# Optimization experiments

Hardware: AMD Instinct MI355X
Metric: run time of the kernel (lower is better)

The kernel has to match this reference:

```python
import jax, jax.numpy as jnp
import numpy as np

B, TA, TV, D, H = 4, 1024, 1024, 512, 8
HD = D // H
SCALE = HD ** -0.5
LN_EPS = 1e-5


def setup_inputs() -> dict:
    key = jax.random.key(0)
    ks = jax.random.split(key, 16)
    init = lambda k, shape, s: (jax.random.normal(k, shape, jnp.float32) * s)
    inp = {
        'q': jax.random.normal(ks[0], (B, TA, D), jnp.float32),
        'k': jax.random.normal(ks[1], (B, TV, D), jnp.float32),
        'v': jax.random.normal(ks[2], (B, TV, D), jnp.float32),
        'guide_map': jax.random.uniform(ks[3], (B, TA, TV), jnp.float32),
        'Wq': init(ks[4], (D, D), D ** -0.5), 'bq': jnp.zeros((D,), jnp.float32),
        'Wk': init(ks[5], (D, D), D ** -0.5), 'bk': jnp.zeros((D,), jnp.float32),
        'Wv': init(ks[6], (D, D), D ** -0.5), 'bv': jnp.zeros((D,), jnp.float32),
        'Wo': init(ks[7], (D, D), D ** -0.5), 'bo': jnp.zeros((D,), jnp.float32),
        'ln_gamma': jnp.ones((D,), jnp.float32),
        'ln_beta': jnp.zeros((D,), jnp.float32),
        'gate': jnp.zeros((1,), jnp.float32),
        'bias_scale': jnp.array(10.0, jnp.float32),
    }
    return inp


def layer_norm(x, gamma, beta):
    mu = jnp.mean(x, axis=-1, keepdims=True)
    var = jnp.mean(jnp.square(x - mu), axis=-1, keepdims=True)
    return (x - mu) * jax.lax.rsqrt(var + LN_EPS) * gamma + beta


def reference(q, k, v, guide_map, Wq, bq, Wk, bk, Wv, bv, Wo, bo, ln_gamma, ln_beta, gate, bias_scale):
    # project and split heads: [B, H, T, hd]
    Q = (q @ Wq.T + bq).reshape(B, TA, H, HD).transpose(0, 2, 1, 3)
    K = (k @ Wk.T + bk).reshape(B, TV, H, HD).transpose(0, 2, 1, 3)
    V = (v @ Wv.T + bv).reshape(B, TV, H, HD).transpose(0, 2, 1, 3)
    scores = jnp.einsum('bhqd,bhkd->bhqk', Q, K) * SCALE
    # transport bias, broadcast over heads (guide_map is [B,Ta,Tv])
    transport_bias = jnp.log(guide_map + 1e-8) * jax.nn.softplus(bias_scale)
    scores = scores + transport_bias[:, None, :, :]
    attn = jax.nn.softmax(scores, axis=-1)  # dropout is identity in eval
    context = jnp.einsum('bhqk,bhkd->bhqd', attn, V)
    context = context.transpose(0, 2, 1, 3).reshape(B, TA, D)
    out = context @ Wo.T + bo
    return layer_norm(q + jax.nn.sigmoid(gate) * out, ln_gamma, ln_beta)
```

## Files before the change

kernel.cpp:

```cpp
#include <hip/hip_runtime.h>
#include <hip/hip_bf16.h>
#include <math.h>

typedef __bf16 bf16_t;
typedef _Float16 hf16_t;
typedef bf16_t bf16x8 __attribute__((ext_vector_type(8)));
typedef hf16_t hf16x8 __attribute__((ext_vector_type(8)));
typedef float f32x4 __attribute__((ext_vector_type(4)));

#define B_  4
#define TA_ 1024
#define TV_ 1024
#define D_  512
#define H_  8
#define HD_ 64
#define SCALE_ 0.125f

__device__ inline void g2l16(const void* g, void* l) {
    __builtin_amdgcn_global_load_lds(
        (const __attribute__((address_space(1))) void*)g,
        (__attribute__((address_space(3))) void*)l, 16, 0, 0);
}

template <int CTRL>
__device__ inline float dppmov(float x) {
    int xi = __float_as_int(x);
    return __int_as_float(__builtin_amdgcn_update_dpp(xi, xi, CTRL, 0xF, 0xF, false));
}
__device__ inline float row16_max(float x) {
    x = fmaxf(x, dppmov<0xB1>(x));
    x = fmaxf(x, dppmov<0x4E>(x));
    x = fmaxf(x, dppmov<0x141>(x));
    x = fmaxf(x, dppmov<0x140>(x));
    return x;
}
__device__ inline float row16_sum(float x) {
    x += dppmov<0xB1>(x);
    x += dppmov<0x4E>(x);
    x += dppmov<0x141>(x);
    x += dppmov<0x140>(x);
    return x;
}

__global__ __launch_bounds__(256) void prep_all(
    const float* __restrict__ G, hf16_t* __restrict__ bias_t,
    const float* __restrict__ q, const float* __restrict__ k, const float* __restrict__ v,
    const float* __restrict__ Wq, const float* __restrict__ Wk,
    const float* __restrict__ Wv, const float* __restrict__ Wo,
    bf16_t* __restrict__ qb, bf16_t* __restrict__ kb, bf16_t* __restrict__ vb,
    bf16_t* __restrict__ Wb)
{
    const int tid = threadIdx.x;
    if (blockIdx.x < 1024) {
        __shared__ float Gt[64][68];
        const int kt = blockIdx.x & 15, q64 = (blockIdx.x >> 4) & 15, b = blockIdx.x >> 8;
        const int row = tid >> 4, col4 = (tid & 15) * 4;
        #pragma unroll
        for (int it = 0; it < 4; ++it) {
            int r = it * 16 + row;
            f32x4 g = *(const f32x4*)(G + ((size_t)(b * TA_ + q64 * 64 + r)) * TV_ + kt * 64 + col4);
            *(f32x4*)&Gt[r][col4] = g;
        }
        __syncthreads();
        const int lane = tid & 63, wave = tid >> 6, quad = lane >> 4, l16 = lane & 15;
        hf16x8 lo, hi;
        #pragma unroll
        for (int ct = 0; ct < 4; ++ct) {
            #pragma unroll
            for (int r = 0; r < 4; ++r) {
                float gv = Gt[wave * 16 + quad * 4 + r][ct * 16 + l16];
                float lb = __logf(gv + 1e-8f);
                int idx = ct * 4 + r;
                if (idx < 8) lo[idx] = (hf16_t)lb; else hi[idx - 8] = (hf16_t)lb;
            }
        }
        size_t doff = ((((size_t)b * 16 + kt) * 16 + q64) * 256 + tid) * 16;
        *(hf16x8*)(bias_t + doff) = lo;
        *(hf16x8*)(bias_t + doff + 8) = hi;
    } else {
        const size_t i = ((size_t)(blockIdx.x - 1024) * 256 + tid) * 8;
        const float* src; bf16_t* dst; size_t off;
        const size_t M2 = (size_t)1 << 21;
        if (i < M2)          { src = q; dst = qb; off = i; }
        else if (i < 2 * M2) { src = k; dst = kb; off = i - M2; }
        else if (i < 3 * M2) { src = v; dst = vb; off = i - 2 * M2; }
        else {
            size_t j = i - 3 * M2;
            int wsel = (int)(j >> 18); off = j & 262143;
            src = (wsel == 0) ? Wq : (wsel == 1) ? Wk : (wsel == 2) ? Wv : Wo;
            dst = Wb + ((size_t)wsel << 18);
        }
        f32x4 a = *(const f32x4*)(src + off), c = *(const f32x4*)(src + off + 4);
        bf16x8 r;
        #pragma unroll
        for (int t = 0; t < 4; ++t) { r[t] = (bf16_t)a[t]; r[t + 4] = (bf16_t)c[t]; }
        *(bf16x8*)(dst + off) = r;
    }
}

__device__ inline void gemm128_core(
    const bf16_t* __restrict__ X, const bf16_t* __restrict__ W,
    int mbase, int nbase, bf16_t (*__restrict__ Asm)[128 * 32],
    bf16_t (*__restrict__ Bsm)[128 * 32], f32x4 acc[4][4])
{
    const int tid  = threadIdx.x;
    const int wave = tid >> 6, lane = tid & 63;
    const int quad = lane >> 4, l16 = lane & 15;
    const int wm = wave & 1, wn = wave >> 1;
    const int srow = lane >> 2;
    const int scol = (lane & 3) * 8;

    auto stage = [&](int kt, int buf) {
        const int k0 = kt * 32;
        #pragma unroll
        for (int i = 0; i < 2; ++i) {
            const int row = wave * 32 + i * 16;
            g2l16(X + (size_t)(mbase + row + srow) * D_ + k0 + scol,
                  &Asm[buf][row * 32] + (size_t)lane * 8);
            g2l16(W + (size_t)(nbase + row + srow) * D_ + k0 + scol,
                  &Bsm[buf][row * 32] + (size_t)lane * 8);
        }
    };

    stage(0, 0);
    __syncthreads();
    for (int kt = 0; kt < 16; ++kt) {
        const int buf = kt & 1;
        if (kt < 15) stage(kt + 1, buf ^ 1);
        bf16x8 af[4], bf_[4];
        #pragma unroll
        for (int t = 0; t < 4; ++t) {
            af[t]  = *(const bf16x8*)&Asm[buf][(wm * 64 + t * 16 + l16) * 32 + quad * 8];
            bf_[t] = *(const bf16x8*)&Bsm[buf][(wn * 64 + t * 16 + l16) * 32 + quad * 8];
        }
        #pragma unroll
        for (int mt = 0; mt < 4; ++mt) {
            #pragma unroll
            for (int nt = 0; nt < 4; ++nt)
                acc[mt][nt] = __builtin_amdgcn_mfma_f32_16x16x32_bf16(af[mt], bf_[nt], acc[mt][nt], 0, 0, 0);
        }
        __syncthreads();
    }
}

__global__ __launch_bounds__(256) void gemm_qkv(
    const bf16_t* __restrict__ qb, const bf16_t* __restrict__ kb, const bf16_t* __restrict__ vb,
    const bf16_t* __restrict__ Wb,
    const float* __restrict__ bq, const float* __restrict__ bk, const float* __restrict__ bv,
    bf16_t* __restrict__ Qp, bf16_t* __restrict__ Kp, bf16_t* __restrict__ Vt)
{
    __shared__ bf16_t Asm[2][128 * 32];
    __shared__ bf16_t Bsm[2][128 * 32];

    const int tid  = threadIdx.x;
    const int wave = tid >> 6, lane = tid & 63;
    const int quad = lane >> 4, l16 = lane & 15;
    const int wm = wave & 1, wn = wave >> 1;
    const int mbase = blockIdx.x * 128, nbase = blockIdx.y * 128;
    const int z = blockIdx.z;

    const bf16_t* X   = (z == 0) ? qb : (z == 1) ? kb : vb;
    const float* bias = (z == 0) ? bq : (z == 1) ? bk : bv;
    const bf16_t* W   = Wb + ((size_t)z << 18);

    f32x4 acc[4][4] = {};
    gemm128_core(X, W, mbase, nbase, Asm, Bsm, acc);

    bf16_t* out = (z == 0) ? Qp : (z == 1) ? Kp : Vt;
    #pragma unroll
    for (int mt = 0; mt < 4; ++mt) {
        #pragma unroll
        for (int nt = 0; nt < 4; ++nt) {
            #pragma unroll
            for (int r = 0; r < 4; ++r) {
                int m = mbase + wm * 64 + mt * 16 + quad * 4 + r;
                int n = nbase + wn * 64 + nt * 16 + l16;
                float val = acc[mt][nt][r] + bias[n];
                int b = m >> 10, t = m & 1023, h = n >> 6, hd = n & 63;
                if (z != 2)
                    out[(((size_t)(b * H_ + h) * TA_) + t) * HD_ + hd] = (bf16_t)val;
                else
                    out[((size_t)(b * H_ + h) * HD_ + hd) * TV_ + t] = (bf16_t)val;
            }
        }
    }
}

__global__ __launch_bounds__(256) void gemm_out(
    const bf16_t* __restrict__ ctx, const bf16_t* __restrict__ Wob,
    const float* __restrict__ bo, bf16_t* __restrict__ op)
{
    __shared__ bf16_t Asm[2][128 * 32];
    __shared__ bf16_t Bsm[2][128 * 32];

    const int tid  = threadIdx.x;
    const int wave = tid >> 6, lane = tid & 63;
    const int quad = lane >> 4, l16 = lane & 15;
    const int wm = wave & 1, wn = wave >> 1;
    const int mbase = blockIdx.x * 128, nbase = blockIdx.y * 128;

    f32x4 acc[4][4] = {};
    gemm128_core(ctx, Wob, mbase, nbase, Asm, Bsm, acc);

    #pragma unroll
    for (int mt = 0; mt < 4; ++mt) {
        #pragma unroll
        for (int nt = 0; nt < 4; ++nt) {
            #pragma unroll
            for (int r = 0; r < 4; ++r) {
                int m = mbase + wm * 64 + mt * 16 + quad * 4 + r;
                int n = nbase + wn * 64 + nt * 16 + l16;
                op[(size_t)m * D_ + n] = (bf16_t)(acc[mt][nt][r] + bo[n]);
            }
        }
    }
}

__global__ __launch_bounds__(256) void attn_kernel(
    const bf16_t* __restrict__ Qp, const bf16_t* __restrict__ Kp,
    const bf16_t* __restrict__ Vt, const hf16_t* __restrict__ bias_t,
    const float* __restrict__ bias_scale,
    bf16_t* __restrict__ Opart, float* __restrict__ mpart, float* __restrict__ lpart)
{
    __shared__ bf16_t Ksm[2][64][72];
    __shared__ bf16_t Vsm[2][64][72];
    __shared__ bf16_t Plds[4][16][72];

    const int tid  = threadIdx.x;
    const int wave = tid >> 6, lane = tid & 63;
    const int quad = lane >> 4, l16 = lane & 15;
    const int bh = blockIdx.x, b = bh >> 3;
    const int q64 = blockIdx.y;
    const int z = blockIdx.z;
    const int t0 = z * 8;
    const int qbase = q64 * 64 + wave * 16;
    const int rsub = lane >> 3, csub = lane & 7;

    const float sp = log1pf(__expf(bias_scale[0]));

    bf16x8 aq[2];
    #pragma unroll
    for (int s = 0; s < 2; ++s)
        aq[s] = *(const bf16x8*)(Qp + ((size_t)bh * TA_ + qbase + l16) * HD_ + s * 32 + quad * 8);

    f32x4 o[4] = {};
    float m_[4], l_[4];
    #pragma unroll
    for (int i = 0; i < 4; ++i) { m_[i] = -1e30f; l_[i] = 0.f; }

    auto issue_kv = [&](int kt, bf16x8 kr[2], bf16x8 vr[2]) {
        const int kbase = kt * 64;
        #pragma unroll
        for (int i = 0; i < 2; ++i) {
            int row = wave * 16 + i * 8 + rsub;
            kr[i] = *(const bf16x8*)(Kp + ((size_t)bh * TV_ + kbase + row) * HD_ + csub * 8);
            vr[i] = *(const bf16x8*)(Vt + ((size_t)bh * HD_ + row) * TV_ + kbase + csub * 8);
        }
    };
    auto write_kv = [&](int buf, bf16x8 kr[2], bf16x8 vr[2]) {
        #pragma unroll
        for (int i = 0; i < 2; ++i) {
            int row = wave * 16 + i * 8 + rsub;
            *(bf16x8*)&Ksm[buf][row][csub * 8] = kr[i];
            *(bf16x8*)&Vsm[buf][row][csub * 8] = vr[i];
        }
    };

    const hf16_t* bias_base = bias_t + (((size_t)b * 16 * 16 + q64) * 256 + tid) * 16;
    auto bias_ld = [&](int kt, hf16x8& lo, hf16x8& hi) {
        const hf16_t* bp = bias_base + (size_t)kt * 65536;
        lo = *(const hf16x8*)bp;
        hi = *(const hf16x8*)(bp + 8);
    };
    hf16x8 b0lo, b0hi, b1lo, b1hi;
    bias_ld(t0, b0lo, b0hi);
    bias_ld(t0 + 1, b1lo, b1hi);

    {
        bf16x8 kr[2], vr[2];
        issue_kv(t0, kr, vr);
        write_kv(0, kr, vr);
    }
    __syncthreads();

    auto tile_body = [&](int lk, int buf, hf16x8& slo, hf16x8& shi) {
        const int kt = t0 + lk;
        bf16x8 krn[2], vrn[2];
        if (lk < 7) issue_kv(kt + 1, krn, vrn);
        hf16x8 clo = slo, chi = shi;
        if (lk < 6) bias_ld(kt + 2, slo, shi);

        f32x4 st[4];
        #pragma unroll
        for (int ct = 0; ct < 4; ++ct) {
            f32x4 acc = {};
            #pragma unroll
            for (int s = 0; s < 2; ++s) {
                bf16x8 bk = *(const bf16x8*)&Ksm[buf][ct * 16 + l16][s * 32 + quad * 8];
                acc = __builtin_amdgcn_mfma_f32_16x16x32_bf16(aq[s], bk, acc, 0, 0, 0);
            }
            st[ct] = acc;
        }
        float sv[4][4], mx[4];
        #pragma unroll
        for (int r = 0; r < 4; ++r) mx[r] = -1e30f;
        #pragma unroll
        for (int ct = 0; ct < 4; ++ct) {
            #pragma unroll
            for (int r = 0; r < 4; ++r) {
                int idx = ct * 4 + r;
                float lb = (idx < 8) ? (float)clo[idx] : (float)chi[idx - 8];
                float val = fmaf(lb, sp, st[ct][r] * SCALE_);
                sv[ct][r] = val;
                mx[r] = fmaxf(mx[r], val);
            }
        }
        float alpha[4];
        #pragma unroll
        for (int r = 0; r < 4; ++r) {
            mx[r] = row16_max(mx[r]);
            float mn = fmaxf(m_[r], mx[r]);
            alpha[r] = __expf(m_[r] - mn);
            m_[r] = mn;
        }
        #pragma unroll
        for (int ct = 0; ct < 4; ++ct) {
            #pragma unroll
            for (int r = 0; r < 4; ++r)
                sv[ct][r] = __expf(sv[ct][r] - m_[r]);
        }
        #pragma unroll
        for (int r = 0; r < 4; ++r) {
            float lsum = row16_sum(sv[0][r] + sv[1][r] + sv[2][r] + sv[3][r]);
            l_[r] = l_[r] * alpha[r] + lsum;
        }
        #pragma unroll
        for (int ct = 0; ct < 4; ++ct) {
            #pragma unroll
            for (int r = 0; r < 4; ++r)
                Plds[wave][quad * 4 + r][ct * 16 + l16] = (bf16_t)sv[ct][r];
        }
        #pragma unroll
        for (int dt = 0; dt < 4; ++dt) {
            #pragma unroll
            for (int r = 0; r < 4; ++r) o[dt][r] *= alpha[r];
        }
        #pragma unroll
        for (int s = 0; s < 2; ++s) {
            bf16x8 ap = *(const bf16x8*)&Plds[wave][l16][s * 32 + quad * 8];
            #pragma unroll
            for (int dt = 0; dt < 4; ++dt) {
                bf16x8 bv = *(const bf16x8*)&Vsm[buf][dt * 16 + l16][s * 32 + quad * 8];
                o[dt] = __builtin_amdgcn_mfma_f32_16x16x32_bf16(ap, bv, o[dt], 0, 0, 0);
            }
        }
        if (lk < 7) write_kv(buf ^ 1, krn, vrn);
        __syncthreads();
    };

    #pragma unroll 1
    for (int kk = 0; kk < 8; kk += 2) {
        tile_body(kk,     0, b0lo, b0hi);
        tile_body(kk + 1, 1, b1lo, b1hi);
    }

    const size_t blk = (size_t)bh * 16 + q64;
    bf16x8 plo, phi;
    #pragma unroll
    for (int dt = 0; dt < 4; ++dt) {
        #pragma unroll
        for (int r = 0; r < 4; ++r) {
            int idx = dt * 4 + r;
            if (idx < 8) plo[idx] = (bf16_t)o[dt][r]; else phi[idx - 8] = (bf16_t)o[dt][r];
        }
    }
    size_t poff = (((size_t)z * 512 + blk) * 256 + tid) * 16;
    *(bf16x8*)(Opart + poff) = plo;
    *(bf16x8*)(Opart + poff + 8) = phi;
    if (l16 == 0) {
        #pragma unroll
        for (int r = 0; r < 4; ++r) {
            int row = wave * 16 + quad * 4 + r;
            mpart[((size_t)z * 512 + blk) * 64 + row] = m_[r];
            lpart[((size_t)z * 512 + blk) * 64 + row] = l_[r];
        }
    }
}

__global__ __launch_bounds__(256) void attn_combine(
    const bf16_t* __restrict__ Opart, const float* __restrict__ mpart,
    const float* __restrict__ lpart, bf16_t* __restrict__ ctx)
{
    const int tid  = threadIdx.x;
    const int wave = tid >> 6, lane = tid & 63;
    const int quad = lane >> 4, l16 = lane & 15;
    const int bh = blockIdx.x, b = bh >> 3, h = bh & 7;
    const int q64 = blockIdx.y;
    const size_t blk = (size_t)bh * 16 + q64;

    size_t p0 = (blk * 256 + tid) * 16;
    size_t p1 = (((size_t)512 + blk) * 256 + tid) * 16;
    bf16x8 a0 = *(const bf16x8*)(Opart + p0), a1 = *(const bf16x8*)(Opart + p0 + 8);
    bf16x8 c0 = *(const bf16x8*)(Opart + p1), c1 = *(const bf16x8*)(Opart + p1 + 8);

    float s0[4], s1[4];
    #pragma unroll
    for (int r = 0; r < 4; ++r) {
        int row = wave * 16 + quad * 4 + r;
        float m0 = mpart[blk * 64 + row], m1 = mpart[(512 + blk) * 64 + row];
        float l0 = lpart[blk * 64 + row], l1 = lpart[(512 + blk) * 64 + row];
        float mm = fmaxf(m0, m1);
        float e0 = __expf(m0 - mm), e1 = __expf(m1 - mm);
        float L = l0 * e0 + l1 * e1;
        s0[r] = e0 / L; s1[r] = e1 / L;
    }
    #pragma unroll
    for (int dt = 0; dt < 4; ++dt) {
        #pragma unroll
        for (int r = 0; r < 4; ++r) {
            int idx = dt * 4 + r;
            float v0 = (idx < 8) ? (float)a0[idx] : (float)a1[idx - 8];
            float v1 = (idx < 8) ? (float)c0[idx] : (float)c1[idx - 8];
            float v = v0 * s0[r] + v1 * s1[r];
            int qrow = q64 * 64 + wave * 16 + quad * 4 + r;
            ctx[((size_t)b * TA_ + qrow) * D_ + h * HD_ + dt * 16 + l16] = (bf16_t)v;
        }
    }
}

__global__ __launch_bounds__(256) void ln_kernel(
    const float* __restrict__ q, const bf16_t* __restrict__ outp,
    const float* __restrict__ gamma, const float* __restrict__ beta,
    const float* __restrict__ gate, float* __restrict__ y)
{
    const int row = blockIdx.x, tid = threadIdx.x;
    const float sg = 1.f / (1.f + __expf(-gate[0]));
    const size_t base = (size_t)row * D_;
    float x0 = q[base + tid]       + sg * (float)outp[base + tid];
    float x1 = q[base + tid + 256] + sg * (float)outp[base + tid + 256];
    float s = x0 + x1, sq = x0 * x0 + x1 * x1;
    #pragma unroll
    for (int off = 1; off < 64; off <<= 1) {
        s  += __shfl_xor(s,  off, 64);
        sq += __shfl_xor(sq, off, 64);
    }
    __shared__ float ss[4], sqq[4];
    if ((tid & 63) == 0) { ss[tid >> 6] = s; sqq[tid >> 6] = sq; }
    __syncthreads();
    s  = ss[0] + ss[1] + ss[2] + ss[3];
    sq = sqq[0] + sqq[1] + sqq[2] + sqq[3];
    const float mu = s * (1.f / D_);
    const float var = sq * (1.f / D_) - mu * mu;
    const float rstd = rsqrtf(var + 1e-5f);
    y[base + tid]       = (x0 - mu) * rstd * gamma[tid] + beta[tid];
    y[base + tid + 256] = (x1 - mu) * rstd * gamma[tid + 256] + beta[tid + 256];
}

extern "C" void kernel_launch(void* const* d_in, const int* in_sizes, int n_in,
                              void* d_out, int out_size, void* d_ws, size_t ws_size,
                              hipStream_t stream) {
    const float* q       = (const float*)d_in[0];
    const float* k       = (const float*)d_in[1];
    const float* v       = (const float*)d_in[2];
    const float* guide   = (const float*)d_in[3];
    const float* Wq      = (const float*)d_in[4];
    const float* bq      = (const float*)d_in[5];
    const float* Wk      = (const float*)d_in[6];
    const float* bk      = (const float*)d_in[7];
    const float* Wv      = (const float*)d_in[8];
    const float* bv      = (const float*)d_in[9];
    const float* Wo      = (const float*)d_in[10];
    const float* bo      = (const float*)d_in[11];
    const float* gamma   = (const float*)d_in[12];
    const float* beta    = (const float*)d_in[13];
    const float* gate    = (const float*)d_in[14];
    const float* bscale  = (const float*)d_in[15];

    char* w = (char*)d_ws;
    bf16_t* qb     = (bf16_t*)(w);
    bf16_t* kb     = (bf16_t*)(w + (4u  << 20));
    bf16_t* vb     = (bf16_t*)(w + (8u  << 20));
    bf16_t* Wb     = (bf16_t*)(w + (12u << 20));
    bf16_t* Qp     = (bf16_t*)(w + (14u << 20));
    bf16_t* Kp     = (bf16_t*)(w + (18u << 20));
    bf16_t* Vt     = (bf16_t*)(w + (22u << 20));
    bf16_t* ctx    = (bf16_t*)(w + (26u << 20));
    hf16_t* bias_t = (hf16_t*)(w + (30u << 20));
    bf16_t* Opart  = (bf16_t*)(w + (38u << 20));
    float*  mpart  = (float*) (w + (46u << 20));
    float*  lpart  = (float*) (w + (47u << 20));
    bf16_t* op     = (bf16_t*)(w);

    prep_all<<<4608, 256, 0, stream>>>(guide, bias_t, q, k, v, Wq, Wk, Wv, Wo, qb, kb, vb, Wb);
    gemm_qkv<<<dim3(32, 4, 3), 256, 0, stream>>>(qb, kb, vb, Wb, bq, bk, bv, Qp, Kp, Vt);
    attn_kernel<<<dim3(32, 16, 2), 256, 0, stream>>>(Qp, Kp, Vt, bias_t, bscale, Opart, mpart, lpart);
    attn_combine<<<dim3(32, 16), 256, 0, stream>>>(Opart, mpart, lpart, ctx);
    gemm_out<<<dim3(32, 4), 256, 0, stream>>>(ctx, Wb + ((size_t)3 << 18), bo, op);
    ln_kernel<<<4096, 256, 0, stream>>>(q, op, gamma, beta, gate, (float*)d_out);
}
```

Baseline: 182.7 us.

## Compute transposed S tile so P stays in registers for PV MFMA

Swaps the MFMA operands in QK^T so each lane holds a column of scores for one query row. Row max and sum then need only two cross-lane shuffles, and P can feed the 16x16x16 MFMA directly from registers, with no round trip through LDS. The bias layout in the prep kernel is transposed to match. The cost is twice as many smaller PV MFMAs, plus per-row shuffles to broadcast alpha onto the output accumulators.

```diff
diff --git a/kernel.cpp b/kernel.cpp
--- a/kernel.cpp
+++ b/kernel.cpp
@@ -5,8 +5,10 @@
 typedef __bf16 bf16_t;
 typedef _Float16 hf16_t;
 typedef bf16_t bf16x8 __attribute__((ext_vector_type(8)));
+typedef bf16_t bf16x4 __attribute__((ext_vector_type(4)));
 typedef hf16_t hf16x8 __attribute__((ext_vector_type(8)));
 typedef float f32x4 __attribute__((ext_vector_type(4)));
+typedef short s16x4 __attribute__((ext_vector_type(4)));
 
 #define B_  4
 #define TA_ 1024
@@ -22,24 +24,9 @@
         (__attribute__((address_space(3))) void*)l, 16, 0, 0);
 }
 
-template <int CTRL>
-__device__ inline float dppmov(float x) {
-    int xi = __float_as_int(x);
-    return __int_as_float(__builtin_amdgcn_update_dpp(xi, xi, CTRL, 0xF, 0xF, false));
-}
-__device__ inline float row16_max(float x) {
-    x = fmaxf(x, dppmov<0xB1>(x));
-    x = fmaxf(x, dppmov<0x4E>(x));
-    x = fmaxf(x, dppmov<0x141>(x));
-    x = fmaxf(x, dppmov<0x140>(x));
-    return x;
-}
-__device__ inline float row16_sum(float x) {
-    x += dppmov<0xB1>(x);
-    x += dppmov<0x4E>(x);
-    x += dppmov<0x141>(x);
-    x += dppmov<0x140>(x);
-    return x;
+__device__ inline f32x4 mfma16_bf16(bf16x4 a, bf16x4 b, f32x4 c) {
+    return __builtin_amdgcn_mfma_f32_16x16x16bf16_1k(
+        __builtin_bit_cast(s16x4, a), __builtin_bit_cast(s16x4, b), c, 0, 0, 0);
 }
 
 __global__ __launch_bounds__(256) void prep_all(
@@ -68,7 +55,7 @@
         for (int ct = 0; ct < 4; ++ct) {
             #pragma unroll
             for (int r = 0; r < 4; ++r) {
-                float gv = Gt[wave * 16 + quad * 4 + r][ct * 16 + l16];
+                float gv = Gt[wave * 16 + l16][ct * 16 + quad * 4 + r];
                 float lb = __logf(gv + 1e-8f);
                 int idx = ct * 4 + r;
                 if (idx < 8) lo[idx] = (hf16_t)lb; else hi[idx - 8] = (hf16_t)lb;
@@ -224,7 +211,6 @@
 {
     __shared__ bf16_t Ksm[2][64][72];
     __shared__ bf16_t Vsm[2][64][72];
-    __shared__ bf16_t Plds[4][16][72];
 
     const int tid  = threadIdx.x;
     const int wave = tid >> 6, lane = tid & 63;
@@ -235,6 +221,7 @@
     const int t0 = z * 8;
     const int qbase = q64 * 64 + wave * 16;
     const int rsub = lane >> 3, csub = lane & 7;
+    const int shsrc = (lane & 48) | ((lane >> 2) & 12);
 
     const float sp = log1pf(__expf(bias_scale[0]));
 
@@ -244,9 +231,7 @@
         aq[s] = *(const bf16x8*)(Qp + ((size_t)bh * TA_ + qbase + l16) * HD_ + s * 32 + quad * 8);
 
     f32x4 o[4] = {};
-    float m_[4], l_[4];
-    #pragma unroll
-    for (int i = 0; i < 4; ++i) { m_[i] = -1e30f; l_[i] = 0.f; }
+    float m_ = -1e30f, l_ = 0.f;
 
     auto issue_kv = [&](int kt, bf16x8 kr[2], bf16x8 vr[2]) {
         const int kbase = kt * 64;
@@ -297,13 +282,11 @@
             #pragma unroll
             for (int s = 0; s < 2; ++s) {
                 bf16x8 bk = *(const bf16x8*)&Ksm[buf][ct * 16 + l16][s * 32 + quad * 8];
-                acc = __builtin_amdgcn_mfma_f32_16x16x32_bf16(aq[s], bk, acc, 0, 0, 0);
+                acc = __builtin_amdgcn_mfma_f32_16x16x32_bf16(bk, aq[s], acc, 0, 0, 0);
             }
             st[ct] = acc;
         }
-        float sv[4][4], mx[4];
-        #pragma unroll
-        for (int r = 0; r < 4; ++r) mx[r] = -1e30f;
+        float sv[4][4], mx = -1e30f;
         #pragma unroll
         for (int ct = 0; ct < 4; ++ct) {
             #pragma unroll
@@ -312,46 +295,42 @@
                 float lb = (idx < 8) ? (float)clo[idx] : (float)chi[idx - 8];
                 float val = fmaf(lb, sp, st[ct][r] * SCALE_);
                 sv[ct][r] = val;
-                mx[r] = fmaxf(mx[r], val);
-            }
-        }
-        float alpha[4];
+                mx = fmaxf(mx, val);
+            }
+        }
+        mx = fmaxf(mx, __shfl_xor(mx, 16, 64));
+        mx = fmaxf(mx, __shfl_xor(mx, 32, 64));
+        float mn = fmaxf(m_, mx);
+        float alpha = __expf(m_ - mn);
+        m_ = mn;
+        float ls = 0.f;
+        #pragma unroll
+        for (int ct = 0; ct < 4; ++ct) {
+            #pragma unroll
+            for (int r = 0; r < 4; ++r) {
+                float p = __expf(sv[ct][r] - mn);
+                sv[ct][r] = p;
+                ls += p;
+            }
+        }
+        ls += __shfl_xor(ls, 16, 64);
+        ls += __shfl_xor(ls, 32, 64);
+        l_ = l_ * alpha + ls;
         #pragma unroll
         for (int r = 0; r < 4; ++r) {
-            mx[r] = row16_max(mx[r]);
-            float mn = fmaxf(m_[r], mx[r]);
-            alpha[r] = __expf(m_[r] - mn);
-            m_[r] = mn;
+            float af = __shfl(alpha, shsrc | r, 64);
+            #pragma unroll
+            for (int dt = 0; dt < 4; ++dt) o[dt][r] *= af;
         }
         #pragma unroll
         for (int ct = 0; ct < 4; ++ct) {
-            #pragma unroll
-            for (int r = 0; r < 4; ++r)
-                sv[ct][r] = __expf(sv[ct][r] - m_[r]);
-        }
-        #pragma unroll
-        for (int r = 0; r < 4; ++r) {
-            float lsum = row16_sum(sv[0][r] + sv[1][r] + sv[2][r] + sv[3][r]);
-            l_[r] = l_[r] * alpha[r] + lsum;
-        }
-        #pragma unroll
-        for (int ct = 0; ct < 4; ++ct) {
-            #pragma unroll
-            for (int r = 0; r < 4; ++r)
-                Plds[wave][quad * 4 + r][ct * 16 + l16] = (bf16_t)sv[ct][r];
-        }
-        #pragma unroll
-        for (int dt = 0; dt < 4; ++dt) {
-            #pragma unroll
-            for (int r = 0; r < 4; ++r) o[dt][r] *= alpha[r];
-        }
-        #pragma unroll
-        for (int s = 0; s < 2; ++s) {
-            bf16x8 ap = *(const bf16x8*)&Plds[wave][l16][s * 32 + quad * 8];
+            bf16x4 ap;
+            #pragma unroll
+            for (int r = 0; r < 4; ++r) ap[r] = (bf16_t)sv[ct][r];
             #pragma unroll
             for (int dt = 0; dt < 4; ++dt) {
-                bf16x8 bv = *(const bf16x8*)&Vsm[buf][dt * 16 + l16][s * 32 + quad * 8];
-                o[dt] = __builtin_amdgcn_mfma_f32_16x16x32_bf16(ap, bv, o[dt], 0, 0, 0);
+                bf16x4 bv = *(const bf16x4*)&Vsm[buf][dt * 16 + l16][ct * 16 + quad * 4];
+                o[dt] = mfma16_bf16(ap, bv, o[dt]);
             }
         }
         if (lk < 7) write_kv(buf ^ 1, krn, vrn);
@@ -377,13 +356,10 @@
     size_t poff = (((size_t)z * 512 + blk) * 256 + tid) * 16;
     *(bf16x8*)(Opart + poff) = plo;
     *(bf16x8*)(Opart + poff + 8) = phi;
-    if (l16 == 0) {
-        #pragma unroll
-        for (int r = 0; r < 4; ++r) {
-            int row = wave * 16 + quad * 4 + r;
-            mpart[((size_t)z * 512 + blk) * 64 + row] = m_[r];
-            lpart[((size_t)z * 512 + blk) * 64 + row] = l_[r];
-        }
+    if (quad == 0) {
+        int row = wave * 16 + l16;
+        mpart[((size_t)z * 512 + blk) * 64 + row] = m_;
+        lpart[((size_t)z * 512 + blk) * 64 + row] = l_;
     }
 }
 
```

New measurement: 181.9 us. About the same (-0.5%).
